# Performance work log

Hardware: AMD Instinct MI355X
Metric: run time of the kernel (lower is better)

Reference implementation:

```python
import jax, jax.numpy as jnp
import numpy as np

N_PL = 16      # PiecewiseLin resolution
OBJECTS = 10   # top-k objects kept / max count


def plin(w, x):
    """PiecewiseLin forward: w is [N_PL+1], x is any-shape tensor in [0,1]."""
    w = jnp.abs(w)
    w = w / w.sum()
    csum = jnp.cumsum(w)                     # [N_PL+1]
    y = N_PL * x
    idx = y.astype(jnp.int32)                # trunc toward zero (x >= 0)
    f = y - jnp.trunc(y)                     # fractional part
    lo = csum[jnp.minimum(idx, N_PL)]
    hi = w[jnp.minimum(idx + 1, N_PL)]
    return lo + f * hi


def _area(box):  # box: [n, 4, o]
    return jnp.clip(box[:, 2] - box[:, 0], 0.0, None) * jnp.clip(box[:, 3] - box[:, 1], 0.0, None)


def _iou(a, b):  # a, b: [n, 4, o] -> [n, o, o]
    mn = jnp.maximum(a[:, :2, :, None], b[:, :2, None, :])
    mx = jnp.minimum(a[:, 2:, :, None], b[:, 2:, None, :])
    wh = jnp.clip(mx - mn, 0.0, None)
    inter = wh[:, 0] * wh[:, 1]
    aa = _area(a)[:, :, None]
    ab = _area(b)[:, None, :]
    return inter / (aa + ab - inter + 1e-12)


def counter_forward(boxes, attention, ws):
    n = boxes.shape[0]
    # filter_most_important: top-k by attention
    att, idx = jax.lax.top_k(attention, OBJECTS)                       # [n, o]
    idx_b = jnp.broadcast_to(idx[:, None, :], (n, 4, OBJECTS))
    boxes = jnp.take_along_axis(boxes, idx_b, axis=2)                  # [n, 4, o]
    att = jax.nn.sigmoid(att)                                          # already_sigmoided=False

    relev = att[:, :, None] * att[:, None, :]                          # [n, o, o]
    dist = 1.0 - _iou(boxes, boxes)                                    # [n, o, o]

    score = plin(ws[0], relev) * plin(ws[1], dist)
    dedup = plin(ws[3], relev) * plin(ws[4], dist)

    # deduplicate
    att_diff = jnp.abs(att[:, :, None] - att[:, None, :])              # [n, o, o]
    score_diff = jnp.abs(dedup[..., :, None] - dedup[..., None, :])    # [n, o, o, o]
    sim = plin(ws[2], 1.0 - score_diff).prod(axis=1) * plin(ws[2], 1.0 - att_diff)  # [n, o, o]
    row_sims = sim.sum(axis=2)                                         # [n, o]
    all_sims = row_sims[:, :, None] * row_sims[:, None, :]             # [n, o, o]

    score = score / all_sims
    correction = plin(ws[0], att * att) / row_sims                     # [n, o]
    total = score.sum(axis=(1, 2))[:, None] + correction.sum(axis=1, keepdims=True)  # [n, 1]
    total = jnp.sqrt(total + 1e-20)

    # to_one_hot
    s = jnp.clip(total, 0.0, float(OBJECTS))                           # [n, 1]
    i = s.astype(jnp.int32)[:, 0]
    f = s - jnp.trunc(s)
    tl = jax.nn.one_hot(jnp.minimum(i, OBJECTS), OBJECTS + 1, dtype=s.dtype)
    tr = jax.nn.one_hot(jnp.minimum(i + 1, OBJECTS), OBJECTS + 1, dtype=s.dtype)
    one_hot = (1.0 - f) * tl + f * tr                                  # [n, o+1]

    # confidence
    att_conf = jnp.abs(plin(ws[5], att) - 0.5)                         # [n, o]
    dist_conf = jnp.abs(plin(ws[6], dist) - 0.5)                       # [n, o, o]
    conf = plin(ws[7], att_conf.mean(axis=1, keepdims=True)
                + dist_conf.mean(axis=2).mean(axis=1, keepdims=True))  # [n, 1]
    return one_hot * conf                                              # [n, o+1]


def setup_inputs() -> dict:
    key = jax.random.key(0)
    k1, k2, k3 = jax.random.split(key, 3)
    n, m = 32768, 36
    boxes = jax.random.uniform(k1, (n, 4, m), dtype=jnp.float32)
    attention = jax.random.normal(k2, (n, m), dtype=jnp.float32)
    ws = jax.random.uniform(k3, (8, N_PL + 1), dtype=jnp.float32, minval=0.1, maxval=1.0)
    return {"boxes": boxes, "attention": attention, "ws": ws}


def reference(boxes, attention, ws):
    return counter_forward(boxes, attention, ws)
```

## Files before the change

### kernel.cpp

```cpp
#include <hip/hip_runtime.h>
#include <math.h>

#define N_PL 16
#define NT   17
#define OBJ  10
#define M    36
#define SPB  4
#define BLK  64
#define CSTR 12

__constant__ unsigned char c_p55[55] = {
 0x00,0x01,0x02,0x03,0x04,0x05,0x06,0x07,0x08,0x09,
 0x11,0x12,0x13,0x14,0x15,0x16,0x17,0x18,0x19,
 0x22,0x23,0x24,0x25,0x26,0x27,0x28,0x29,
 0x33,0x34,0x35,0x36,0x37,0x38,0x39,
 0x44,0x45,0x46,0x47,0x48,0x49,
 0x55,0x56,0x57,0x58,0x59,
 0x66,0x67,0x68,0x69,
 0x77,0x78,0x79,
 0x88,0x89,
 0x99};
__constant__ unsigned char c_p45[45] = {
 0x01,0x02,0x03,0x04,0x05,0x06,0x07,0x08,0x09,
 0x12,0x13,0x14,0x15,0x16,0x17,0x18,0x19,
 0x23,0x24,0x25,0x26,0x27,0x28,0x29,
 0x34,0x35,0x36,0x37,0x38,0x39,
 0x45,0x46,0x47,0x48,0x49,
 0x56,0x57,0x58,0x59,
 0x67,0x68,0x69,
 0x78,0x79,
 0x89};

__device__ __forceinline__ float plin2(const float2* tb, float x) {
    float y = 16.0f * x;
    int idx = (int)y;
    float f = y - (float)idx;
    int i0 = idx < N_PL ? idx : N_PL;
    float2 cw = tb[i0];
    return __builtin_fmaf(f, cw.y, cw.x);
}

__device__ __forceinline__ unsigned long long mkkey(float v, int m) {
    unsigned int b = __float_as_uint(v);
    unsigned int u = b ^ (0x80000000u | (unsigned int)((int)b >> 31));
    return ((unsigned long long)u << 6) | (unsigned int)(63 - m);
}

__global__ __launch_bounds__(BLK, 4) void counter_kernel(
    const float* __restrict__ boxes,
    const float* __restrict__ attn,
    const float* __restrict__ ws,
    float* __restrict__ out,
    int n)
{
    __shared__ float2 s_tab2[8 * NT];
    __shared__ float4 s_bx[SPB][OBJ];
    __shared__ float2 s_aa[SPB][OBJ];
    __shared__ float  s_ded[SPB][CSTR * OBJ];
    __shared__ float  s_sim[SPB][CSTR * OBJ];
    __shared__ float  s_rf[SPB][OBJ];

    const int tid = threadIdx.x;
    const int g = tid & 15;
    const int p = tid >> 4;

    if (tid < 8) {
        float w[NT]; float sum = 0.f;
        #pragma unroll
        for (int k = 0; k < NT; ++k) { w[k] = fabsf(ws[tid * NT + k]); sum += w[k]; }
        float rs = 1.f / sum;
        float wn[NT];
        #pragma unroll
        for (int k = 0; k < NT; ++k) wn[k] = w[k] * rs;
        float c = 0.f;
        #pragma unroll
        for (int k = 0; k < NT; ++k) {
            c += wn[k];
            s_tab2[tid * NT + k] = make_float2(c, wn[k < N_PL ? k + 1 : N_PL]);
        }
    }

    int s = blockIdx.x * SPB + p;
    const bool active = (s < n);
    if (!active) s = n - 1;

    const float* arow = attn + (size_t)s * M;
    float mv[3]; unsigned long long myk[3];
    #pragma unroll
    for (int k = 0; k < 3; ++k) {
        int e = g + 16 * k;
        bool ok = e < M;
        float v = ok ? arow[e] : 0.f;
        mv[k] = v;
        myk[k] = ok ? mkkey(v, e) : 0ull;
    }
    int rnk0 = 0, rnk1 = 0, rnk2 = 0;
    #pragma unroll
    for (int c4 = 0; c4 < 9; ++c4) {
        float4 t4 = ((const float4*)arow)[c4];
        float vv[4] = {t4.x, t4.y, t4.z, t4.w};
        #pragma unroll
        for (int q = 0; q < 4; ++q) {
            unsigned long long kk = mkkey(vv[q], 4 * c4 + q);
            rnk0 += (kk > myk[0]) ? 1 : 0;
            rnk1 += (kk > myk[1]) ? 1 : 0;
            rnk2 += (kk > myk[2]) ? 1 : 0;
        }
    }
    int rnk[3] = {rnk0, rnk1, rnk2};

    __syncthreads();

    const float* brow = boxes + (size_t)s * (4 * M);
    float mA = 0.f;
    #pragma unroll
    for (int k = 0; k < 3; ++k) {
        int e = g + 16 * k;
        if (e < M && rnk[k] < OBJ) {
            float a = 1.f / (1.f + __expf(-mv[k]));
            int r = rnk[k];
            mA += fabsf(plin2(s_tab2 + 5 * NT, a) - 0.5f);
            float x0 = brow[e], y0 = brow[M + e], x1 = brow[2 * M + e], y1 = brow[3 * M + e];
            s_bx[p][r] = make_float4(x0, y0, x1, y1);
            s_aa[p][r] = make_float2(a, fmaxf(x1 - x0, 0.f) * fmaxf(y1 - y0, 0.f));
        }
    }
    __syncthreads();

    float mD = 0.f;
    float sc_loc[4];
    int pkA[4];
    #pragma unroll
    for (int t = 0; t < 4; ++t) {
        int q = g + 16 * t;
        bool act = (q < 55);
        int pk = c_p55[act ? q : 0];
        pkA[t] = pk;
        int i = pk >> 4, j = pk & 15;
        float4 bi = s_bx[p][i], bj = s_bx[p][j];
        float2 ai = s_aa[p][i], aj = s_aa[p][j];
        float wx = fminf(bi.z, bj.z) - fmaxf(bi.x, bj.x);
        float wy = fminf(bi.w, bj.w) - fmaxf(bi.y, bj.y);
        float inter = fmaxf(wx, 0.f) * fmaxf(wy, 0.f);
        float un = ai.y + aj.y - inter + 1e-12f;
        float d = 1.f - inter * __builtin_amdgcn_rcpf(un);
        float relev = ai.x * aj.x;
        float dd = plin2(s_tab2 + 3 * NT, relev) * plin2(s_tab2 + 4 * NT, d);
        sc_loc[t] = plin2(s_tab2 + 0 * NT, relev) * plin2(s_tab2 + 1 * NT, d);
        float dc = fabsf(plin2(s_tab2 + 6 * NT, d) - 0.5f);
        if (act) {
            s_ded[p][i * CSTR + j] = dd;
            s_ded[p][j * CSTR + i] = dd;
            mD += (i != j) ? 2.f * dc : dc;
        }
    }
    __syncthreads();

    if (g < OBJ) s_sim[p][g * CSTR + g] = 0.f;
    #pragma unroll
    for (int t = 0; t < 3; ++t) {
        int q = g + 16 * t;
        bool act = (q < 45);
        int pk = c_p45[act ? q : 0];
        int i = pk >> 4, j = pk & 15;
        float2 ai = s_aa[p][i], aj = s_aa[p][j];
        float prod = plin2(s_tab2 + 2 * NT, 1.f - fabsf(ai.x - aj.x));
        const float* ci = &s_ded[p][i * CSTR];
        const float* cj = &s_ded[p][j * CSTR];
        float4 ci0 = *(const float4*)ci;
        float4 ci1 = *(const float4*)(ci + 4);
        float2 ci2 = *(const float2*)(ci + 8);
        float4 cj0 = *(const float4*)cj;
        float4 cj1 = *(const float4*)(cj + 4);
        float2 cj2 = *(const float2*)(cj + 8);
        const float2* tb2 = s_tab2 + 2 * NT;
        prod *= plin2(tb2, 1.f - fabsf(ci0.x - cj0.x));
        prod *= plin2(tb2, 1.f - fabsf(ci0.y - cj0.y));
        prod *= plin2(tb2, 1.f - fabsf(ci0.z - cj0.z));
        prod *= plin2(tb2, 1.f - fabsf(ci0.w - cj0.w));
        prod *= plin2(tb2, 1.f - fabsf(ci1.x - cj1.x));
        prod *= plin2(tb2, 1.f - fabsf(ci1.y - cj1.y));
        prod *= plin2(tb2, 1.f - fabsf(ci1.z - cj1.z));
        prod *= plin2(tb2, 1.f - fabsf(ci1.w - cj1.w));
        prod *= plin2(tb2, 1.f - fabsf(ci2.x - cj2.x));
        prod *= plin2(tb2, 1.f - fabsf(ci2.y - cj2.y));
        if (act) {
            s_sim[p][i * CSTR + j] = prod;
            s_sim[p][j * CSTR + i] = prod;
        }
    }
    __syncthreads();

    if (g < OBJ) {
        float c16 = s_tab2[2 * NT + N_PL].x;
        float c2 = c16 * c16, c4 = c2 * c2, c8 = c4 * c4;
        float diag = c8 * c2 * c16;
        const float* rw = &s_sim[p][g * CSTR];
        float4 r0 = *(const float4*)rw;
        float4 r1 = *(const float4*)(rw + 4);
        float2 r2 = *(const float2*)(rw + 8);
        float sum = diag + r0.x + r0.y + r0.z + r0.w
                         + r1.x + r1.y + r1.z + r1.w + r2.x + r2.y;
        s_rf[p][g] = 1.f / sum;
    }
    __syncthreads();

    float tot = 0.f;
    #pragma unroll
    for (int t = 0; t < 4; ++t) {
        int q = g + 16 * t;
        bool act = (q < 55);
        int pk = pkA[t];
        int i = pk >> 4, j = pk & 15;
        float term = sc_loc[t] * s_rf[p][i] * s_rf[p][j];
        if (act) tot += (i != j) ? 2.f * term : term;
    }
    if (g < OBJ) {
        float ai = s_aa[p][g].x;
        tot += plin2(s_tab2 + 0 * NT, ai * ai) * s_rf[p][g];
    }
    float carg = mA * 0.1f + mD * 0.01f;
    tot  += __shfl_xor(tot, 1);  tot  += __shfl_xor(tot, 2);
    tot  += __shfl_xor(tot, 4);  tot  += __shfl_xor(tot, 8);
    carg += __shfl_xor(carg, 1); carg += __shfl_xor(carg, 2);
    carg += __shfl_xor(carg, 4); carg += __shfl_xor(carg, 8);

    float total = sqrtf(tot + 1e-20f);
    float conf = plin2(s_tab2 + 7 * NT, carg);
    float scl = fminf(fmaxf(total, 0.f), 10.f);
    int i0 = (int)scl;
    float f = scl - (float)i0;
    int lo = i0 < OBJ ? i0 : OBJ;
    int hi = (i0 + 1) < OBJ ? (i0 + 1) : OBJ;

    if (active && g <= OBJ) {
        float vv = ((g == lo) ? (1.f - f) : 0.f) + ((g == hi) ? f : 0.f);
        out[(size_t)s * (OBJ + 1) + g] = vv * conf;
    }
}

extern "C" void kernel_launch(void* const* d_in, const int* in_sizes, int n_in,
                              void* d_out, int out_size, void* d_ws, size_t ws_size,
                              hipStream_t stream) {
    const float* boxes = (const float*)d_in[0];
    const float* attn  = (const float*)d_in[1];
    const float* ws    = (const float*)d_in[2];
    float* out = (float*)d_out;
    int n = in_sizes[1] / M;
    int blocks = (n + SPB - 1) / SPB;
    hipLaunchKernelGGL(counter_kernel, dim3(blocks), dim3(BLK), 0, stream,
                       boxes, attn, ws, out, n);
}
```

Before: 86.30 us.

## Hoist global loads before table setup and rank top-k via shared keys

```diff
diff --git a/kernel.cpp b/kernel.cpp
--- a/kernel.cpp
+++ b/kernel.cpp
@@ -31,19 +31,25 @@
  0x78,0x79,
  0x89};
 
-__device__ __forceinline__ float plin2(const float2* tb, float x) {
-    float y = 16.0f * x;
+__device__ __forceinline__ float plinY(const float2* tb, float y) {
     int idx = (int)y;
     float f = y - (float)idx;
-    int i0 = idx < N_PL ? idx : N_PL;
-    float2 cw = tb[i0];
+    float2 cw = tb[idx];
+    return __builtin_fmaf(f, cw.y, cw.x);
+}
+
+__device__ __forceinline__ float plinD(const float2* tb, float a, float b) {
+    float y = __builtin_fmaf(-fabsf(a - b), 16.f, 16.f);
+    int idx = (int)y;
+    float f = y - (float)idx;
+    float2 cw = tb[idx];
     return __builtin_fmaf(f, cw.y, cw.x);
 }
 
 __device__ __forceinline__ unsigned long long mkkey(float v, int m) {
     unsigned int b = __float_as_uint(v);
     unsigned int u = b ^ (0x80000000u | (unsigned int)((int)b >> 31));
-    return ((unsigned long long)u << 6) | (unsigned int)(63 - m);
+    return ((unsigned long long)u << 32) | (unsigned int)(63 - m);
 }
 
 __global__ __launch_bounds__(BLK, 4) void counter_kernel(
@@ -55,7 +61,8 @@
 {
     __shared__ float2 s_tab2[8 * NT];
     __shared__ float4 s_bx[SPB][OBJ];
-    __shared__ float2 s_aa[SPB][OBJ];
+    __shared__ float4 s_aa[SPB][OBJ];
+    __shared__ __align__(16) unsigned long long s_key[SPB][M];
     __shared__ float  s_ded[SPB][CSTR * OBJ];
     __shared__ float  s_sim[SPB][CSTR * OBJ];
     __shared__ float  s_rf[SPB][OBJ];
@@ -63,6 +70,32 @@
     const int tid = threadIdx.x;
     const int g = tid & 15;
     const int p = tid >> 4;
+
+    int s = blockIdx.x * SPB + p;
+    const bool active = (s < n);
+    if (!active) s = n - 1;
+
+    const float* arow = attn + (size_t)s * M;
+    const float* brow = boxes + (size_t)s * (4 * M);
+
+    float mv0 = arow[g];
+    float mv1 = arow[g + 16];
+    float mv2 = (g < 4) ? arow[g + 32] : 0.f;
+
+    float bx0[4], bx1[4], bx2[4];
+    #pragma unroll
+    for (int r = 0; r < 4; ++r) bx0[r] = brow[r * M + g];
+    #pragma unroll
+    for (int r = 0; r < 4; ++r) bx1[r] = brow[r * M + g + 16];
+    #pragma unroll
+    for (int r = 0; r < 4; ++r) bx2[r] = (g < 4) ? brow[r * M + g + 32] : 0.f;
+
+    unsigned long long k0 = mkkey(mv0, g);
+    unsigned long long k1 = mkkey(mv1, g + 16);
+    unsigned long long k2 = (g < 4) ? mkkey(mv2, g + 32) : 0ull;
+    s_key[p][g] = k0;
+    s_key[p][g + 16] = k1;
+    if (g < 4) s_key[p][g + 32] = k2;
 
     if (tid < 8) {
         float w[NT]; float sum = 0.f;
@@ -79,75 +112,74 @@
             s_tab2[tid * NT + k] = make_float2(c, wn[k < N_PL ? k + 1 : N_PL]);
         }
     }
-
-    int s = blockIdx.x * SPB + p;
-    const bool active = (s < n);
-    if (!active) s = n - 1;
-
-    const float* arow = attn + (size_t)s * M;
-    float mv[3]; unsigned long long myk[3];
-    #pragma unroll
-    for (int k = 0; k < 3; ++k) {
-        int e = g + 16 * k;
-        bool ok = e < M;
-        float v = ok ? arow[e] : 0.f;
-        mv[k] = v;
-        myk[k] = ok ? mkkey(v, e) : 0ull;
-    }
-    int rnk0 = 0, rnk1 = 0, rnk2 = 0;
-    #pragma unroll
-    for (int c4 = 0; c4 < 9; ++c4) {
-        float4 t4 = ((const float4*)arow)[c4];
-        float vv[4] = {t4.x, t4.y, t4.z, t4.w};
-        #pragma unroll
-        for (int q = 0; q < 4; ++q) {
-            unsigned long long kk = mkkey(vv[q], 4 * c4 + q);
-            rnk0 += (kk > myk[0]) ? 1 : 0;
-            rnk1 += (kk > myk[1]) ? 1 : 0;
-            rnk2 += (kk > myk[2]) ? 1 : 0;
-        }
-    }
-    int rnk[3] = {rnk0, rnk1, rnk2};
-
-    __syncthreads();
-
-    const float* brow = boxes + (size_t)s * (4 * M);
+    __syncthreads();
+
+    int r0 = 0, r1 = 0, r2 = 0;
+    const ulonglong2* kp = (const ulonglong2*)(&s_key[p][0]);
+    #pragma unroll
+    for (int w = 0; w < 18; ++w) {
+        ulonglong2 kk = kp[w];
+        r0 += (kk.x > k0); r0 += (kk.y > k0);
+        r1 += (kk.x > k1); r1 += (kk.y > k1);
+        r2 += (kk.x > k2); r2 += (kk.y > k2);
+    }
+
     float mA = 0.f;
-    #pragma unroll
-    for (int k = 0; k < 3; ++k) {
-        int e = g + 16 * k;
-        if (e < M && rnk[k] < OBJ) {
-            float a = 1.f / (1.f + __expf(-mv[k]));
-            int r = rnk[k];
-            mA += fabsf(plin2(s_tab2 + 5 * NT, a) - 0.5f);
-            float x0 = brow[e], y0 = brow[M + e], x1 = brow[2 * M + e], y1 = brow[3 * M + e];
-            s_bx[p][r] = make_float4(x0, y0, x1, y1);
-            s_aa[p][r] = make_float2(a, fmaxf(x1 - x0, 0.f) * fmaxf(y1 - y0, 0.f));
-        }
+    if (r0 < OBJ) {
+        float a = 1.f / (1.f + __expf(-mv0));
+        float a16 = 16.f * a;
+        mA += fabsf(plinY(s_tab2 + 5 * NT, a16) - 0.5f);
+        s_bx[p][r0] = make_float4(bx0[0], bx0[1], bx0[2], bx0[3]);
+        s_aa[p][r0] = make_float4(a,
+            fmaxf(bx0[2] - bx0[0], 0.f) * fmaxf(bx0[3] - bx0[1], 0.f), a16, 0.f);
+    }
+    if (r1 < OBJ) {
+        float a = 1.f / (1.f + __expf(-mv1));
+        float a16 = 16.f * a;
+        mA += fabsf(plinY(s_tab2 + 5 * NT, a16) - 0.5f);
+        s_bx[p][r1] = make_float4(bx1[0], bx1[1], bx1[2], bx1[3]);
+        s_aa[p][r1] = make_float4(a,
+            fmaxf(bx1[2] - bx1[0], 0.f) * fmaxf(bx1[3] - bx1[1], 0.f), a16, 0.f);
+    }
+    if (r2 < OBJ) {
+        float a = 1.f / (1.f + __expf(-mv2));
+        float a16 = 16.f * a;
+        mA += fabsf(plinY(s_tab2 + 5 * NT, a16) - 0.5f);
+        s_bx[p][r2] = make_float4(bx2[0], bx2[1], bx2[2], bx2[3]);
+        s_aa[p][r2] = make_float4(a,
+            fmaxf(bx2[2] - bx2[0], 0.f) * fmaxf(bx2[3] - bx2[1], 0.f), a16, 0.f);
     }
     __syncthreads();
 
     float mD = 0.f;
     float sc_loc[4];
-    int pkA[4];
+    unsigned int pks = 0;
     #pragma unroll
     for (int t = 0; t < 4; ++t) {
         int q = g + 16 * t;
         bool act = (q < 55);
         int pk = c_p55[act ? q : 0];
-        pkA[t] = pk;
+        pks |= (unsigned int)pk << (8 * t);
         int i = pk >> 4, j = pk & 15;
         float4 bi = s_bx[p][i], bj = s_bx[p][j];
-        float2 ai = s_aa[p][i], aj = s_aa[p][j];
+        float4 ai = s_aa[p][i], aj = s_aa[p][j];
         float wx = fminf(bi.z, bj.z) - fmaxf(bi.x, bj.x);
         float wy = fminf(bi.w, bj.w) - fmaxf(bi.y, bj.y);
         float inter = fmaxf(wx, 0.f) * fmaxf(wy, 0.f);
         float un = ai.y + aj.y - inter + 1e-12f;
-        float d = 1.f - inter * __builtin_amdgcn_rcpf(un);
-        float relev = ai.x * aj.x;
-        float dd = plin2(s_tab2 + 3 * NT, relev) * plin2(s_tab2 + 4 * NT, d);
-        sc_loc[t] = plin2(s_tab2 + 0 * NT, relev) * plin2(s_tab2 + 1 * NT, d);
-        float dc = fabsf(plin2(s_tab2 + 6 * NT, d) - 0.5f);
+        float iou = inter * __builtin_amdgcn_rcpf(un);
+        float yd = __builtin_fmaf(iou, -16.f, 16.f);
+        int id_ = (int)yd; float fd = yd - (float)id_;
+        float yr = ai.z * aj.x;
+        int ir_ = (int)yr; float fr = yr - (float)ir_;
+        float2 c0 = s_tab2[ir_];
+        float2 c1 = s_tab2[NT + id_];
+        float2 c3 = s_tab2[3 * NT + ir_];
+        float2 c4 = s_tab2[4 * NT + id_];
+        float2 c6 = s_tab2[6 * NT + id_];
+        sc_loc[t] = __builtin_fmaf(fr, c0.y, c0.x) * __builtin_fmaf(fd, c1.y, c1.x);
+        float dd  = __builtin_fmaf(fr, c3.y, c3.x) * __builtin_fmaf(fd, c4.y, c4.x);
+        float dc  = fabsf(__builtin_fmaf(fd, c6.y, c6.x) - 0.5f);
         if (act) {
             s_ded[p][i * CSTR + j] = dd;
             s_ded[p][j * CSTR + i] = dd;
@@ -163,8 +195,9 @@
         bool act = (q < 45);
         int pk = c_p45[act ? q : 0];
         int i = pk >> 4, j = pk & 15;
-        float2 ai = s_aa[p][i], aj = s_aa[p][j];
-        float prod = plin2(s_tab2 + 2 * NT, 1.f - fabsf(ai.x - aj.x));
+        float4 ai = s_aa[p][i], aj = s_aa[p][j];
+        const float2* tb2 = s_tab2 + 2 * NT;
+        float prod = plinD(tb2, ai.x, aj.x);
         const float* ci = &s_ded[p][i * CSTR];
         const float* cj = &s_ded[p][j * CSTR];
         float4 ci0 = *(const float4*)ci;
@@ -173,17 +206,16 @@
         float4 cj0 = *(const float4*)cj;
         float4 cj1 = *(const float4*)(cj + 4);
         float2 cj2 = *(const float2*)(cj + 8);
-        const float2* tb2 = s_tab2 + 2 * NT;
-        prod *= plin2(tb2, 1.f - fabsf(ci0.x - cj0.x));
-        prod *= plin2(tb2, 1.f - fabsf(ci0.y - cj0.y));
-        prod *= plin2(tb2, 1.f - fabsf(ci0.z - cj0.z));
-        prod *= plin2(tb2, 1.f - fabsf(ci0.w - cj0.w));
-        prod *= plin2(tb2, 1.f - fabsf(ci1.x - cj1.x));
-        prod *= plin2(tb2, 1.f - fabsf(ci1.y - cj1.y));
-        prod *= plin2(tb2, 1.f - fabsf(ci1.z - cj1.z));
-        prod *= plin2(tb2, 1.f - fabsf(ci1.w - cj1.w));
-        prod *= plin2(tb2, 1.f - fabsf(ci2.x - cj2.x));
-        prod *= plin2(tb2, 1.f - fabsf(ci2.y - cj2.y));
+        prod *= plinD(tb2, ci0.x, cj0.x);
+        prod *= plinD(tb2, ci0.y, cj0.y);
+        prod *= plinD(tb2, ci0.z, cj0.z);
+        prod *= plinD(tb2, ci0.w, cj0.w);
+        prod *= plinD(tb2, ci1.x, cj1.x);
+        prod *= plinD(tb2, ci1.y, cj1.y);
+        prod *= plinD(tb2, ci1.z, cj1.z);
+        prod *= plinD(tb2, ci1.w, cj1.w);
+        prod *= plinD(tb2, ci2.x, cj2.x);
+        prod *= plinD(tb2, ci2.y, cj2.y);
         if (act) {
             s_sim[p][i * CSTR + j] = prod;
             s_sim[p][j * CSTR + i] = prod;
@@ -196,11 +228,11 @@
         float c2 = c16 * c16, c4 = c2 * c2, c8 = c4 * c4;
         float diag = c8 * c2 * c16;
         const float* rw = &s_sim[p][g * CSTR];
-        float4 r0 = *(const float4*)rw;
-        float4 r1 = *(const float4*)(rw + 4);
-        float2 r2 = *(const float2*)(rw + 8);
-        float sum = diag + r0.x + r0.y + r0.z + r0.w
-                         + r1.x + r1.y + r1.z + r1.w + r2.x + r2.y;
+        float4 q0 = *(const float4*)rw;
+        float4 q1 = *(const float4*)(rw + 4);
+        float2 q2 = *(const float2*)(rw + 8);
+        float sum = diag + q0.x + q0.y + q0.z + q0.w
+                         + q1.x + q1.y + q1.z + q1.w + q2.x + q2.y;
         s_rf[p][g] = 1.f / sum;
     }
     __syncthreads();
@@ -210,23 +242,24 @@
     for (int t = 0; t < 4; ++t) {
         int q = g + 16 * t;
         bool act = (q < 55);
-        int pk = pkA[t];
+        int pk = (int)((pks >> (8 * t)) & 255u);
         int i = pk >> 4, j = pk & 15;
         float term = sc_loc[t] * s_rf[p][i] * s_rf[p][j];
         if (act) tot += (i != j) ? 2.f * term : term;
     }
     if (g < OBJ) {
-        float ai = s_aa[p][g].x;
-        tot += plin2(s_tab2 + 0 * NT, ai * ai) * s_rf[p][g];
-    }
-    float carg = mA * 0.1f + mD * 0.01f;
-    tot  += __shfl_xor(tot, 1);  tot  += __shfl_xor(tot, 2);
-    tot  += __shfl_xor(tot, 4);  tot  += __shfl_xor(tot, 8);
-    carg += __shfl_xor(carg, 1); carg += __shfl_xor(carg, 2);
-    carg += __shfl_xor(carg, 4); carg += __shfl_xor(carg, 8);
+        float4 aa = s_aa[p][g];
+        float y = aa.z * aa.x;
+        tot += plinY(s_tab2, y) * s_rf[p][g];
+    }
+    float carg16 = __builtin_fmaf(mD, 0.16f, mA * 1.6f);
+    tot    += __shfl_xor(tot, 1);    tot    += __shfl_xor(tot, 2);
+    tot    += __shfl_xor(tot, 4);    tot    += __shfl_xor(tot, 8);
+    carg16 += __shfl_xor(carg16, 1); carg16 += __shfl_xor(carg16, 2);
+    carg16 += __shfl_xor(carg16, 4); carg16 += __shfl_xor(carg16, 8);
 
     float total = sqrtf(tot + 1e-20f);
-    float conf = plin2(s_tab2 + 7 * NT, carg);
+    float conf = plinY(s_tab2 + 7 * NT, carg16);
     float scl = fminf(fmaxf(total, 0.f), 10.f);
     int i0 = (int)scl;
     float f = scl - (float)i0;
```

Result: no change. 84.65 us (-1.9%).
